# Kernel tuning notes

Hardware: AMD Instinct MI355X
Metric: run time of the kernel (lower is better)

The kernel has to match this reference:

```python
import jax, jax.numpy as jnp
import numpy as np

N, E = 50000, 800000
D_IN, D_DEG, D_H, D_UP = 96, 32, 256, 128
EPS = 0.0  # non-trainable buffer, initial_eps=0


def setup_inputs() -> dict:
    key = jax.random.key(0)
    ks = jax.random.split(key, 8)
    d = D_IN + D_DEG  # 128, feature dim after degree-as-tag concat
    return {
        "x": jax.random.normal(ks[0], (N, D_IN), dtype=jnp.float32),
        "degrees": jax.random.uniform(ks[1], (N, D_DEG), dtype=jnp.float32),
        "edge_features": jax.random.normal(ks[2], (E, d), dtype=jnp.float32),
        "W1": jax.random.normal(ks[3], (d, D_H), dtype=jnp.float32) * (1.0 / np.sqrt(d)),
        "b1": jnp.zeros((D_H,), dtype=jnp.float32),
        "W2": jax.random.normal(ks[4], (D_H, D_UP), dtype=jnp.float32) * (1.0 / np.sqrt(D_H)),
        "b2": jnp.zeros((D_UP,), dtype=jnp.float32),
        "edge_index": jax.random.randint(ks[5], (2, E), 0, N, dtype=jnp.int64),
    }


def reference(x, degrees, edge_features, W1, b1, W2, b2, edge_index):
    # degree_as_tag + retain_features: concat node features with degree tags
    h = jnp.concatenate([x, degrees], axis=-1)  # [N, 128]
    # flow='source_to_target': source j = edge_index[0], target i = edge_index[1]
    src, dst = edge_index[0], edge_index[1]
    msgs = jax.nn.relu(h[src] + edge_features)  # [E, 128]
    agg = jax.ops.segment_sum(msgs, dst, num_segments=N)  # [N, 128]
    z = (1.0 + EPS) * h + agg
    # update MLP: Linear -> ReLU -> Linear
    out = jax.nn.relu(z @ W1 + b1) @ W2 + b2  # [N, 128]
    return out
```

## Files before the change

### kernel.cpp

```cpp
#include <hip/hip_runtime.h>


constexpr int DIN  = 96;
constexpr int DDEG = 32;
constexpr int D    = 128;
constexpr int DH   = 256;
constexpr int DUP  = 128;

typedef short bf16x8 __attribute__((ext_vector_type(8)));
typedef float f32x4  __attribute__((ext_vector_type(4)));

static __device__ __forceinline__ ushort f2bf(float f) {
    unsigned u = __float_as_uint(f);
    unsigned r = (u + 0x7fff + ((u >> 16) & 1)) >> 16;
    return (ushort)r;
}
static __device__ __forceinline__ float4 bf4_to_f4(ushort4 u) {
    float4 r;
    r.x = __uint_as_float((unsigned)u.x << 16);
    r.y = __uint_as_float((unsigned)u.y << 16);
    r.z = __uint_as_float((unsigned)u.z << 16);
    r.w = __uint_as_float((unsigned)u.w << 16);
    return r;
}

static __device__ __forceinline__ int waveInclScan(int v, int lane) {
#pragma unroll
    for (int off = 1; off < 64; off <<= 1) {
        int t = __shfl_up(v, off, 64);
        if (lane >= off) v += t;
    }
    return v;
}

__global__ __launch_bounds__(256) void init_h_kernel(
    const float* __restrict__ x, const float* __restrict__ deg,
    ushort* __restrict__ hp, int* __restrict__ counts, int N) {
    int t = blockIdx.x * 256 + threadIdx.x;
    if (t < (N >> 2)) *reinterpret_cast<int4*>(&counts[t * 4]) = make_int4(0, 0, 0, 0);
    if (t == (N >> 2) && (N & 3)) {
        for (int i = (N & ~3); i < N; ++i) counts[i] = 0;
    }
    if (t >= N * 32) return;
    int n = t >> 5, c = t & 31;
    float4 v;
    if (c < 24) v = *reinterpret_cast<const float4*>(&x[(size_t)n * DIN + c * 4]);
    else        v = *reinterpret_cast<const float4*>(&deg[(size_t)n * DDEG + (c - 24) * 4]);
    ushort4 o;
    o.x = f2bf(v.x); o.y = f2bf(v.y); o.z = f2bf(v.z); o.w = f2bf(v.w);
    *reinterpret_cast<ushort4*>(&hp[(size_t)n * D + c * 4]) = o;
}

__global__ __launch_bounds__(256) void count_kernel(
    const int* __restrict__ ei, int* __restrict__ counts, int N, int E) {
    int e = blockIdx.x * 256 + threadIdx.x;
    if (e >= E) return;
    atomicAdd(&counts[ei[E + e]], 1);
}

__global__ __launch_bounds__(256) void scan_partial_kernel(
    const int* __restrict__ counts, int* __restrict__ blockSums, int N) {
    const int tid = threadIdx.x;
    int base = blockIdx.x * 1024 + tid * 4;
    int4 c = make_int4(0, 0, 0, 0);
    if (base + 3 < N) c = *reinterpret_cast<const int4*>(&counts[base]);
    else if (base < N) {
        c.x = counts[base];
        if (base + 1 < N) c.y = counts[base + 1];
        if (base + 2 < N) c.z = counts[base + 2];
    }
    int s = c.x + c.y + c.z + c.w;
#pragma unroll
    for (int off = 32; off; off >>= 1) s += __shfl_xor(s, off, 64);
    __shared__ int wsum[4];
    if ((tid & 63) == 0) wsum[tid >> 6] = s;
    __syncthreads();
    if (tid == 0) blockSums[blockIdx.x] = wsum[0] + wsum[1] + wsum[2] + wsum[3];
}

__global__ __launch_bounds__(64) void scan_base_kernel(
    const int* __restrict__ blockSums, int* __restrict__ blockBase, int nb) {
    int l = threadIdx.x;
    int orig = (l < nb) ? blockSums[l] : 0;
    int incl = waveInclScan(orig, l);
    if (l < nb) blockBase[l] = incl - orig;
}

__global__ __launch_bounds__(256) void scan_final_kernel(
    const int* __restrict__ counts, const int* __restrict__ blockBase,
    int* __restrict__ offsets, int* __restrict__ cursor, int N, int E) {
    const int tid = threadIdx.x, lane = tid & 63, wave = tid >> 6;
    int base = blockIdx.x * 1024 + tid * 4;
    int4 c = make_int4(0, 0, 0, 0);
    if (base + 3 < N) c = *reinterpret_cast<const int4*>(&counts[base]);
    else if (base < N) {
        c.x = counts[base];
        if (base + 1 < N) c.y = counts[base + 1];
        if (base + 2 < N) c.z = counts[base + 2];
    }
    int s = c.x + c.y + c.z + c.w;
    int incl = waveInclScan(s, lane);
    __shared__ int wsum[4];
    if (lane == 63) wsum[wave] = incl;
    __syncthreads();
    int wb = 0;
#pragma unroll
    for (int w = 0; w < 4; ++w)
        if (w < wave) wb += wsum[w];
    int ex = blockBase[blockIdx.x] + wb + (incl - s);
    if (base < N)     { offsets[base]     = ex; cursor[base]     = ex; } ex += c.x;
    if (base + 1 < N) { offsets[base + 1] = ex; cursor[base + 1] = ex; } ex += c.y;
    if (base + 2 < N) { offsets[base + 2] = ex; cursor[base + 2] = ex; } ex += c.z;
    if (base + 3 < N) { offsets[base + 3] = ex; cursor[base + 3] = ex; }
    if (blockIdx.x == 0 && tid == 0) offsets[N] = E;
}

__global__ __launch_bounds__(256) void fill_kernel(
    const int* __restrict__ ei, int* __restrict__ cursor,
    int2* __restrict__ eids2, int E) {
    int e = blockIdx.x * 256 + threadIdx.x;
    if (e >= E) return;
    int src = ei[e];
    int dst = ei[E + e];
    int pos = atomicAdd(&cursor[dst], 1);
    eids2[pos] = make_int2(e, src);
}

__global__ __launch_bounds__(256) void gather_kernel(
    const ushort* __restrict__ hp, const float* __restrict__ ef,
    const int* __restrict__ offsets, const int2* __restrict__ eids2,
    ushort* __restrict__ zb, int N) {
    const int node = blockIdx.x * 8 + (threadIdx.x >> 5);
    if (node >= N) return;
    const int c = threadIdx.x & 31;

    float4 h = bf4_to_f4(*reinterpret_cast<const ushort4*>(&hp[(size_t)node * D + c * 4]));

    float4 acc = make_float4(0.f, 0.f, 0.f, 0.f);
    const int pEnd = offsets[node + 1];
    int p = offsets[node];

    for (; p + 4 <= pEnd; p += 4) {
        int2 i0 = eids2[p + 0];
        int2 i1 = eids2[p + 1];
        int2 i2 = eids2[p + 2];
        int2 i3 = eids2[p + 3];
        f32x4 f0 = __builtin_nontemporal_load(
            reinterpret_cast<const f32x4*>(&ef[(size_t)i0.x * D + c * 4]));
        f32x4 f1 = __builtin_nontemporal_load(
            reinterpret_cast<const f32x4*>(&ef[(size_t)i1.x * D + c * 4]));
        f32x4 f2 = __builtin_nontemporal_load(
            reinterpret_cast<const f32x4*>(&ef[(size_t)i2.x * D + c * 4]));
        f32x4 f3 = __builtin_nontemporal_load(
            reinterpret_cast<const f32x4*>(&ef[(size_t)i3.x * D + c * 4]));
        float4 h0 = bf4_to_f4(*reinterpret_cast<const ushort4*>(&hp[(size_t)i0.y * D + c * 4]));
        float4 h1 = bf4_to_f4(*reinterpret_cast<const ushort4*>(&hp[(size_t)i1.y * D + c * 4]));
        float4 h2 = bf4_to_f4(*reinterpret_cast<const ushort4*>(&hp[(size_t)i2.y * D + c * 4]));
        float4 h3 = bf4_to_f4(*reinterpret_cast<const ushort4*>(&hp[(size_t)i3.y * D + c * 4]));
        acc.x += fmaxf(f0[0] + h0.x, 0.f) + fmaxf(f1[0] + h1.x, 0.f)
               + fmaxf(f2[0] + h2.x, 0.f) + fmaxf(f3[0] + h3.x, 0.f);
        acc.y += fmaxf(f0[1] + h0.y, 0.f) + fmaxf(f1[1] + h1.y, 0.f)
               + fmaxf(f2[1] + h2.y, 0.f) + fmaxf(f3[1] + h3.y, 0.f);
        acc.z += fmaxf(f0[2] + h0.z, 0.f) + fmaxf(f1[2] + h1.z, 0.f)
               + fmaxf(f2[2] + h2.z, 0.f) + fmaxf(f3[2] + h3.z, 0.f);
        acc.w += fmaxf(f0[3] + h0.w, 0.f) + fmaxf(f1[3] + h1.w, 0.f)
               + fmaxf(f2[3] + h2.w, 0.f) + fmaxf(f3[3] + h3.w, 0.f);
    }
    for (; p < pEnd; ++p) {
        int2 i0 = eids2[p];
        f32x4 f0 = __builtin_nontemporal_load(
            reinterpret_cast<const f32x4*>(&ef[(size_t)i0.x * D + c * 4]));
        float4 h0 = bf4_to_f4(*reinterpret_cast<const ushort4*>(&hp[(size_t)i0.y * D + c * 4]));
        acc.x += fmaxf(f0[0] + h0.x, 0.f);
        acc.y += fmaxf(f0[1] + h0.y, 0.f);
        acc.z += fmaxf(f0[2] + h0.z, 0.f);
        acc.w += fmaxf(f0[3] + h0.w, 0.f);
    }
    ushort4 o;
    o.x = f2bf(h.x + acc.x);
    o.y = f2bf(h.y + acc.y);
    o.z = f2bf(h.z + acc.z);
    o.w = f2bf(h.w + acc.w);
    *reinterpret_cast<ushort4*>(&zb[(size_t)node * D + c * 4]) = o;
}

__global__ __launch_bounds__(256) void pack_w_kernel(
    const float* __restrict__ W1, const float* __restrict__ W2,
    ushort* __restrict__ w1p, ushort* __restrict__ w2p) {
    int idx = blockIdx.x * 256 + threadIdx.x;
    if (idx >= 32768) return;
    {
        int j = idx & 7, l = (idx >> 3) & 63, nb = (idx >> 9) & 15, kb = idx >> 13;
        int k = kb * 32 + (l >> 4) * 8 + j, n = nb * 16 + (l & 15);
        w1p[idx] = f2bf(W1[k * DH + n]);
    }
    {
        int j = idx & 7, l = (idx >> 3) & 63, nb = (idx >> 9) & 7, kb = idx >> 12;
        int k = kb * 32 + (l >> 4) * 8 + j, n = nb * 16 + (l & 15);
        w2p[idx] = f2bf(W2[k * DUP + n]);
    }
}

__global__ __launch_bounds__(256) void mlp_mfma_kernel(
    const ushort* __restrict__ zb,
    const ushort* __restrict__ w1p, const float* __restrict__ b1,
    const ushort* __restrict__ w2p, const float* __restrict__ b2,
    float* __restrict__ out, int N) {
    __shared__ ushort u_lds[4][16][DH + 8];
    const int tid = threadIdx.x;
    const int wave = tid >> 6, lane = tid & 63;
    const int m0 = blockIdx.x * 64 + wave * 16;
    const int lr = lane & 15, lg = lane >> 4;

    bf16x8 a1[4];
    int rowA = m0 + lr; if (rowA > N - 1) rowA = N - 1;
    const ushort* zrow = &zb[(size_t)rowA * D + lg * 8];
#pragma unroll
    for (int kb = 0; kb < 4; ++kb)
        a1[kb] = *reinterpret_cast<const bf16x8*>(zrow + kb * 32);

#pragma unroll
    for (int nb = 0; nb < 16; ++nb) {
        f32x4 c = {0.f, 0.f, 0.f, 0.f};
#pragma unroll
        for (int kb = 0; kb < 4; ++kb) {
            bf16x8 b = *reinterpret_cast<const bf16x8*>(&w1p[((kb * 16 + nb) * 64 + lane) * 8]);
            c = __builtin_amdgcn_mfma_f32_16x16x32_bf16(a1[kb], b, c, 0, 0, 0);
        }
        float bias = b1[nb * 16 + lr];
#pragma unroll
        for (int r = 0; r < 4; ++r) {
            float v = fmaxf(c[r] + bias, 0.f);
            u_lds[wave][lg * 4 + r][nb * 16 + lr] = f2bf(v);
        }
    }
    __syncthreads();

    bf16x8 a2[8];
#pragma unroll
    for (int kb = 0; kb < 8; ++kb)
        a2[kb] = *reinterpret_cast<const bf16x8*>(&u_lds[wave][lr][kb * 32 + lg * 8]);

#pragma unroll
    for (int nb = 0; nb < 8; ++nb) {
        f32x4 c = {0.f, 0.f, 0.f, 0.f};
#pragma unroll
        for (int kb = 0; kb < 8; ++kb) {
            bf16x8 b = *reinterpret_cast<const bf16x8*>(&w2p[((kb * 8 + nb) * 64 + lane) * 8]);
            c = __builtin_amdgcn_mfma_f32_16x16x32_bf16(a2[kb], b, c, 0, 0, 0);
        }
        float bias = b2[nb * 16 + lr];
#pragma unroll
        for (int r = 0; r < 4; ++r) {
            int row = m0 + lg * 4 + r;
            if (row < N) out[(size_t)row * DUP + nb * 16 + lr] = c[r] + bias;
        }
    }
}

extern "C" void kernel_launch(void* const* d_in, const int* in_sizes, int n_in,
                              void* d_out, int out_size, void* d_ws, size_t ws_size,
                              hipStream_t stream) {
    const float* x   = (const float*)d_in[0];
    const float* dg  = (const float*)d_in[1];
    const float* ef  = (const float*)d_in[2];
    const float* W1  = (const float*)d_in[3];
    const float* b1  = (const float*)d_in[4];
    const float* W2  = (const float*)d_in[5];
    const float* b2  = (const float*)d_in[6];
    const int*   ei  = (const int*)d_in[7];
    float* out = (float*)d_out;

    const int N = in_sizes[0] / DIN;
    const int E = in_sizes[7] / 2;

    auto align16 = [](size_t v) { return (v + 15) & ~(size_t)15; };
    char* w = (char*)d_ws;
    ushort* zb      = (ushort*)w;  w += align16((size_t)N * D * 2);
    ushort* hp      = (ushort*)w;  w += align16((size_t)N * D * 2);
    int*   counts   = (int*)w;     w += align16((size_t)N * 4);
    int*   offsets  = (int*)w;     w += align16((size_t)(N + 1) * 4);
    int*   cursor   = (int*)w;     w += align16((size_t)N * 4);
    int2*  eids2    = (int2*)w;    w += align16((size_t)E * 8);
    int*   blockSums= (int*)w;     w += align16(64 * 4);
    int*   blockBase= (int*)w;     w += align16(64 * 4);
    ushort* w1p     = (ushort*)w;  w += align16((size_t)D * DH * 2);
    ushort* w2p     = (ushort*)w;  w += align16((size_t)DH * DUP * 2);

    const int eb = (E + 255) / 256;
    const int nbScan = (N + 1023) / 1024;

    init_h_kernel<<<(N * 32 + 255) / 256, 256, 0, stream>>>(x, dg, hp, counts, N);
    count_kernel<<<eb, 256, 0, stream>>>(ei, counts, N, E);
    scan_partial_kernel<<<nbScan, 256, 0, stream>>>(counts, blockSums, N);
    scan_base_kernel<<<1, 64, 0, stream>>>(blockSums, blockBase, nbScan);
    scan_final_kernel<<<nbScan, 256, 0, stream>>>(counts, blockBase, offsets, cursor, N, E);
    fill_kernel<<<eb, 256, 0, stream>>>(ei, cursor, eids2, E);

    gather_kernel<<<(N + 7) / 8, 256, 0, stream>>>(hp, ef, offsets, eids2, zb, N);

    pack_w_kernel<<<128, 256, 0, stream>>>(W1, W2, w1p, w2p);
    mlp_mfma_kernel<<<(N + 63) / 64, 256, 0, stream>>>(zb, w1p, b1, w2p, b2, out, N);
}
```

Measured before the change: 242.7 us.

## Fuse neighbor gather into MLP kernel via LDS and fold weight packing into init

Merges the gather/aggregate kernel with the MFMA MLP kernel: each 256-thread block aggregates 64 nodes into shared memory, then runs both matmuls from LDS, removing the zb global round trip and one launch. Weight packing moves into the init kernel, removing another launch. In exchange the grid shrinks from 6250 to 782 blocks for the latency-bound gather phase, and each half-wave now walks 8 nodes serially, which may reduce memory-level parallelism.

```diff
diff --git a/kernel.cpp b/kernel.cpp
--- a/kernel.cpp
+++ b/kernel.cpp
@@ -9,13 +9,14 @@
 
 typedef short bf16x8 __attribute__((ext_vector_type(8)));
 typedef float f32x4  __attribute__((ext_vector_type(4)));
+typedef unsigned short u16x4 __attribute__((ext_vector_type(4)));
 
 static __device__ __forceinline__ ushort f2bf(float f) {
     unsigned u = __float_as_uint(f);
     unsigned r = (u + 0x7fff + ((u >> 16) & 1)) >> 16;
     return (ushort)r;
 }
-static __device__ __forceinline__ float4 bf4_to_f4(ushort4 u) {
+static __device__ __forceinline__ float4 bfv_to_f4(u16x4 u) {
     float4 r;
     r.x = __uint_as_float((unsigned)u.x << 16);
     r.y = __uint_as_float((unsigned)u.y << 16);
@@ -35,20 +36,32 @@
 
 __global__ __launch_bounds__(256) void init_h_kernel(
     const float* __restrict__ x, const float* __restrict__ deg,
-    ushort* __restrict__ hp, int* __restrict__ counts, int N) {
+    const float* __restrict__ W1, const float* __restrict__ W2,
+    ushort* __restrict__ hp, ushort* __restrict__ w1p, ushort* __restrict__ w2p,
+    int* __restrict__ counts, int N) {
     int t = blockIdx.x * 256 + threadIdx.x;
     if (t < (N >> 2)) *reinterpret_cast<int4*>(&counts[t * 4]) = make_int4(0, 0, 0, 0);
     if (t == (N >> 2) && (N & 3)) {
         for (int i = (N & ~3); i < N; ++i) counts[i] = 0;
+    }
+    if (t < 32768) {
+        {
+            int j = t & 7, l = (t >> 3) & 63, nb = (t >> 9) & 15, kb = t >> 13;
+            w1p[t] = f2bf(W1[(kb * 32 + (l >> 4) * 8 + j) * DH + nb * 16 + (l & 15)]);
+        }
+        {
+            int j = t & 7, l = (t >> 3) & 63, nb = (t >> 9) & 7, kb = t >> 12;
+            w2p[t] = f2bf(W2[(kb * 32 + (l >> 4) * 8 + j) * DUP + nb * 16 + (l & 15)]);
+        }
     }
     if (t >= N * 32) return;
     int n = t >> 5, c = t & 31;
     float4 v;
     if (c < 24) v = *reinterpret_cast<const float4*>(&x[(size_t)n * DIN + c * 4]);
     else        v = *reinterpret_cast<const float4*>(&deg[(size_t)n * DDEG + (c - 24) * 4]);
-    ushort4 o;
+    u16x4 o;
     o.x = f2bf(v.x); o.y = f2bf(v.y); o.z = f2bf(v.z); o.w = f2bf(v.w);
-    *reinterpret_cast<ushort4*>(&hp[(size_t)n * D + c * 4]) = o;
+    *reinterpret_cast<u16x4*>(&hp[(size_t)n * D + c * 4]) = o;
 }
 
 __global__ __launch_bounds__(256) void count_kernel(
@@ -126,98 +139,83 @@
     eids2[pos] = make_int2(e, src);
 }
 
-__global__ __launch_bounds__(256) void gather_kernel(
+__global__ __launch_bounds__(256) void gather_mlp_kernel(
     const ushort* __restrict__ hp, const float* __restrict__ ef,
     const int* __restrict__ offsets, const int2* __restrict__ eids2,
-    ushort* __restrict__ zb, int N) {
-    const int node = blockIdx.x * 8 + (threadIdx.x >> 5);
-    if (node >= N) return;
-    const int c = threadIdx.x & 31;
-
-    float4 h = bf4_to_f4(*reinterpret_cast<const ushort4*>(&hp[(size_t)node * D + c * 4]));
-
-    float4 acc = make_float4(0.f, 0.f, 0.f, 0.f);
-    const int pEnd = offsets[node + 1];
-    int p = offsets[node];
-
-    for (; p + 4 <= pEnd; p += 4) {
-        int2 i0 = eids2[p + 0];
-        int2 i1 = eids2[p + 1];
-        int2 i2 = eids2[p + 2];
-        int2 i3 = eids2[p + 3];
-        f32x4 f0 = __builtin_nontemporal_load(
-            reinterpret_cast<const f32x4*>(&ef[(size_t)i0.x * D + c * 4]));
-        f32x4 f1 = __builtin_nontemporal_load(
-            reinterpret_cast<const f32x4*>(&ef[(size_t)i1.x * D + c * 4]));
-        f32x4 f2 = __builtin_nontemporal_load(
-            reinterpret_cast<const f32x4*>(&ef[(size_t)i2.x * D + c * 4]));
-        f32x4 f3 = __builtin_nontemporal_load(
-            reinterpret_cast<const f32x4*>(&ef[(size_t)i3.x * D + c * 4]));
-        float4 h0 = bf4_to_f4(*reinterpret_cast<const ushort4*>(&hp[(size_t)i0.y * D + c * 4]));
-        float4 h1 = bf4_to_f4(*reinterpret_cast<const ushort4*>(&hp[(size_t)i1.y * D + c * 4]));
-        float4 h2 = bf4_to_f4(*reinterpret_cast<const ushort4*>(&hp[(size_t)i2.y * D + c * 4]));
-        float4 h3 = bf4_to_f4(*reinterpret_cast<const ushort4*>(&hp[(size_t)i3.y * D + c * 4]));
-        acc.x += fmaxf(f0[0] + h0.x, 0.f) + fmaxf(f1[0] + h1.x, 0.f)
-               + fmaxf(f2[0] + h2.x, 0.f) + fmaxf(f3[0] + h3.x, 0.f);
-        acc.y += fmaxf(f0[1] + h0.y, 0.f) + fmaxf(f1[1] + h1.y, 0.f)
-               + fmaxf(f2[1] + h2.y, 0.f) + fmaxf(f3[1] + h3.y, 0.f);
-        acc.z += fmaxf(f0[2] + h0.z, 0.f) + fmaxf(f1[2] + h1.z, 0.f)
-               + fmaxf(f2[2] + h2.z, 0.f) + fmaxf(f3[2] + h3.z, 0.f);
-        acc.w += fmaxf(f0[3] + h0.w, 0.f) + fmaxf(f1[3] + h1.w, 0.f)
-               + fmaxf(f2[3] + h2.w, 0.f) + fmaxf(f3[3] + h3.w, 0.f);
-    }
-    for (; p < pEnd; ++p) {
-        int2 i0 = eids2[p];
-        f32x4 f0 = __builtin_nontemporal_load(
-            reinterpret_cast<const f32x4*>(&ef[(size_t)i0.x * D + c * 4]));
-        float4 h0 = bf4_to_f4(*reinterpret_cast<const ushort4*>(&hp[(size_t)i0.y * D + c * 4]));
-        acc.x += fmaxf(f0[0] + h0.x, 0.f);
-        acc.y += fmaxf(f0[1] + h0.y, 0.f);
-        acc.z += fmaxf(f0[2] + h0.z, 0.f);
-        acc.w += fmaxf(f0[3] + h0.w, 0.f);
-    }
-    ushort4 o;
-    o.x = f2bf(h.x + acc.x);
-    o.y = f2bf(h.y + acc.y);
-    o.z = f2bf(h.z + acc.z);
-    o.w = f2bf(h.w + acc.w);
-    *reinterpret_cast<ushort4*>(&zb[(size_t)node * D + c * 4]) = o;
-}
-
-__global__ __launch_bounds__(256) void pack_w_kernel(
-    const float* __restrict__ W1, const float* __restrict__ W2,
-    ushort* __restrict__ w1p, ushort* __restrict__ w2p) {
-    int idx = blockIdx.x * 256 + threadIdx.x;
-    if (idx >= 32768) return;
-    {
-        int j = idx & 7, l = (idx >> 3) & 63, nb = (idx >> 9) & 15, kb = idx >> 13;
-        int k = kb * 32 + (l >> 4) * 8 + j, n = nb * 16 + (l & 15);
-        w1p[idx] = f2bf(W1[k * DH + n]);
-    }
-    {
-        int j = idx & 7, l = (idx >> 3) & 63, nb = (idx >> 9) & 7, kb = idx >> 12;
-        int k = kb * 32 + (l >> 4) * 8 + j, n = nb * 16 + (l & 15);
-        w2p[idx] = f2bf(W2[k * DUP + n]);
-    }
-}
-
-__global__ __launch_bounds__(256) void mlp_mfma_kernel(
-    const ushort* __restrict__ zb,
     const ushort* __restrict__ w1p, const float* __restrict__ b1,
     const ushort* __restrict__ w2p, const float* __restrict__ b2,
     float* __restrict__ out, int N) {
+    __shared__ ushort zs[64][D];
     __shared__ ushort u_lds[4][16][DH + 8];
     const int tid = threadIdx.x;
+    const int m0 = blockIdx.x * 64;
+
+    {
+        const int hw = tid >> 5, c = tid & 31;
+        for (int i = 0; i < 8; ++i) {
+            int nl = hw * 8 + i;
+            int node = m0 + nl;
+            if (node >= N) break;
+            float4 h = bfv_to_f4(*reinterpret_cast<const u16x4*>(&hp[(size_t)node * D + c * 4]));
+            float4 acc = make_float4(0.f, 0.f, 0.f, 0.f);
+            const int pEnd = offsets[node + 1];
+            int p = offsets[node];
+            for (; p + 4 <= pEnd; p += 4) {
+                int2 i0 = eids2[p + 0];
+                int2 i1 = eids2[p + 1];
+                int2 i2 = eids2[p + 2];
+                int2 i3 = eids2[p + 3];
+                f32x4 f0 = __builtin_nontemporal_load(
+                    reinterpret_cast<const f32x4*>(&ef[(size_t)i0.x * D + c * 4]));
+                f32x4 f1 = __builtin_nontemporal_load(
+                    reinterpret_cast<const f32x4*>(&ef[(size_t)i1.x * D + c * 4]));
+                f32x4 f2 = __builtin_nontemporal_load(
+                    reinterpret_cast<const f32x4*>(&ef[(size_t)i2.x * D + c * 4]));
+                f32x4 f3 = __builtin_nontemporal_load(
+                    reinterpret_cast<const f32x4*>(&ef[(size_t)i3.x * D + c * 4]));
+                float4 h0 = bfv_to_f4(*reinterpret_cast<const u16x4*>(&hp[(size_t)i0.y * D + c * 4]));
+                float4 h1 = bfv_to_f4(*reinterpret_cast<const u16x4*>(&hp[(size_t)i1.y * D + c * 4]));
+                float4 h2 = bfv_to_f4(*reinterpret_cast<const u16x4*>(&hp[(size_t)i2.y * D + c * 4]));
+                float4 h3 = bfv_to_f4(*reinterpret_cast<const u16x4*>(&hp[(size_t)i3.y * D + c * 4]));
+                acc.x += fmaxf(f0[0] + h0.x, 0.f) + fmaxf(f1[0] + h1.x, 0.f)
+                       + fmaxf(f2[0] + h2.x, 0.f) + fmaxf(f3[0] + h3.x, 0.f);
+                acc.y += fmaxf(f0[1] + h0.y, 0.f) + fmaxf(f1[1] + h1.y, 0.f)
+                       + fmaxf(f2[1] + h2.y, 0.f) + fmaxf(f3[1] + h3.y, 0.f);
+                acc.z += fmaxf(f0[2] + h0.z, 0.f) + fmaxf(f1[2] + h1.z, 0.f)
+                       + fmaxf(f2[2] + h2.z, 0.f) + fmaxf(f3[2] + h3.z, 0.f);
+                acc.w += fmaxf(f0[3] + h0.w, 0.f) + fmaxf(f1[3] + h1.w, 0.f)
+                       + fmaxf(f2[3] + h2.w, 0.f) + fmaxf(f3[3] + h3.w, 0.f);
+            }
+            for (; p < pEnd; ++p) {
+                int2 i0 = eids2[p];
+                f32x4 f0 = __builtin_nontemporal_load(
+                    reinterpret_cast<const f32x4*>(&ef[(size_t)i0.x * D + c * 4]));
+                float4 h0 = bfv_to_f4(*reinterpret_cast<const u16x4*>(&hp[(size_t)i0.y * D + c * 4]));
+                acc.x += fmaxf(f0[0] + h0.x, 0.f);
+                acc.y += fmaxf(f0[1] + h0.y, 0.f);
+                acc.z += fmaxf(f0[2] + h0.z, 0.f);
+                acc.w += fmaxf(f0[3] + h0.w, 0.f);
+            }
+            u16x4 o;
+            o.x = f2bf(h.x + acc.x);
+            o.y = f2bf(h.y + acc.y);
+            o.z = f2bf(h.z + acc.z);
+            o.w = f2bf(h.w + acc.w);
+            *reinterpret_cast<u16x4*>(&zs[nl][c * 4]) = o;
+        }
+    }
+    __syncthreads();
+
     const int wave = tid >> 6, lane = tid & 63;
-    const int m0 = blockIdx.x * 64 + wave * 16;
     const int lr = lane & 15, lg = lane >> 4;
+    const int m0w = m0 + wave * 16;
 
     bf16x8 a1[4];
-    int rowA = m0 + lr; if (rowA > N - 1) rowA = N - 1;
-    const ushort* zrow = &zb[(size_t)rowA * D + lg * 8];
+    int lrow = wave * 16 + lr;
+    if (m0 + lrow > N - 1) lrow = N - 1 - m0;
 #pragma unroll
     for (int kb = 0; kb < 4; ++kb)
-        a1[kb] = *reinterpret_cast<const bf16x8*>(zrow + kb * 32);
+        a1[kb] = *reinterpret_cast<const bf16x8*>(&zs[lrow][kb * 32 + lg * 8]);
 
 #pragma unroll
     for (int nb = 0; nb < 16; ++nb) {
@@ -252,7 +250,7 @@
         float bias = b2[nb * 16 + lr];
 #pragma unroll
         for (int r = 0; r < 4; ++r) {
-            int row = m0 + lg * 4 + r;
+            int row = m0w + lg * 4 + r;
             if (row < N) out[(size_t)row * DUP + nb * 16 + lr] = c[r] + bias;
         }
     }
@@ -276,7 +274,6 @@
 
     auto align16 = [](size_t v) { return (v + 15) & ~(size_t)15; };
     char* w = (char*)d_ws;
-    ushort* zb      = (ushort*)w;  w += align16((size_t)N * D * 2);
     ushort* hp      = (ushort*)w;  w += align16((size_t)N * D * 2);
     int*   counts   = (int*)w;     w += align16((size_t)N * 4);
     int*   offsets  = (int*)w;     w += align16((size_t)(N + 1) * 4);
@@ -290,15 +287,14 @@
     const int eb = (E + 255) / 256;
     const int nbScan = (N + 1023) / 1024;
 
-    init_h_kernel<<<(N * 32 + 255) / 256, 256, 0, stream>>>(x, dg, hp, counts, N);
+    init_h_kernel<<<(N * 32 + 255) / 256, 256, 0, stream>>>(
+        x, dg, W1, W2, hp, w1p, w2p, counts, N);
     count_kernel<<<eb, 256, 0, stream>>>(ei, counts, N, E);
     scan_partial_kernel<<<nbScan, 256, 0, stream>>>(counts, blockSums, N);
     scan_base_kernel<<<1, 64, 0, stream>>>(blockSums, blockBase, nbScan);
     scan_final_kernel<<<nbScan, 256, 0, stream>>>(counts, blockBase, offsets, cursor, N, E);
     fill_kernel<<<eb, 256, 0, stream>>>(ei, cursor, eids2, E);
 
-    gather_kernel<<<(N + 7) / 8, 256, 0, stream>>>(hp, ef, offsets, eids2, zb, N);
-
-    pack_w_kernel<<<128, 256, 0, stream>>>(W1, W2, w1p, w2p);
-    mlp_mfma_kernel<<<(N + 63) / 64, 256, 0, stream>>>(zb, w1p, b1, w2p, b2, out, N);
-}
+    gather_mlp_kernel<<<(N + 63) / 64, 256, 0, stream>>>(
+        hp, ef, offsets, eids2, w1p, b1, w2p, b2, out, N);
+}
```

Result: slower. 285.1 us (+17.5%).
